# Optimization experiments

Hardware: AMD Instinct MI355X
Metric: run time of the kernel (lower is better)

## Reference

```python
import jax, jax.numpy as jnp
import numpy as np

B, LONG, SHORT, D, NH, HD = 512, 1000, 50, 64, 4, 16
NUM_ITEMS, TOPK = 100000, 50
NBUCKETS, HASHL, HASHD = 1024, 4, 16  # NOTE: 4 hash layers of D//4 so concat matches item_dim (source default 3 is a shape bug)


def lin(x, w, b):
    return x @ w.T + b


def ln(x, g, b):
    m = x.mean(-1, keepdims=True)
    v = ((x - m) ** 2).mean(-1, keepdims=True)
    return (x - m) / jnp.sqrt(v + 1e-5) * g + b


def setup_inputs() -> dict:
    key = jax.random.key(0)
    ks = jax.random.split(key, 24)
    rn = lambda i, s: jax.random.normal(ks[i], s, jnp.float32) * 0.02
    emb = rn(0, (NUM_ITEMS + 1, D)).at[0].set(0.0)  # padding_idx=0 row zeroed
    return dict(
        user_features=jax.random.normal(ks[1], (B, D), jnp.float32),
        target_item_id=jax.random.randint(ks[2], (B,), 0, NUM_ITEMS + 1),
        short_hist_ids=jax.random.randint(ks[3], (B, SHORT), 0, NUM_ITEMS + 1),
        long_hist_ids=jax.random.randint(ks[4], (B, LONG), 0, NUM_ITEMS + 1),
        item_emb=emb,
        tproj_w=rn(5, (D, D)), tproj_b=jnp.zeros((D,), jnp.float32),
        attn_w1=rn(6, (64, 3 * D)), attn_b1=jnp.zeros((64,), jnp.float32),
        attn_w2=rn(7, (1, 64)), attn_b2=jnp.zeros((1,), jnp.float32),
        hash_emb=rn(8, (HASHL, NBUCKETS, HASHD)),
        sdim_w=rn(9, (D, D)), sdim_b=jnp.zeros((D,), jnp.float32),
        tf_qkv_w=rn(10, (2, 3 * D, D)), tf_qkv_b=jnp.zeros((2, 3 * D), jnp.float32),
        tf_out_w=rn(11, (2, D, D)), tf_out_b=jnp.zeros((2, D), jnp.float32),
        tf_ln1_g=jnp.ones((2, D), jnp.float32), tf_ln1_b=jnp.zeros((2, D), jnp.float32),
        tf_ff1_w=rn(12, (2, 2 * D, D)), tf_ff1_b=jnp.zeros((2, 2 * D), jnp.float32),
        tf_ff2_w=rn(13, (2, D, 2 * D)), tf_ff2_b=jnp.zeros((2, D), jnp.float32),
        tf_ln2_g=jnp.ones((2, D), jnp.float32), tf_ln2_b=jnp.zeros((2, D), jnp.float32),
        fus_w1=rn(14, (256, 4 * D)), fus_b1=jnp.zeros((256,), jnp.float32),
        fus_w2=rn(15, (128, 256)), fus_b2=jnp.zeros((128,), jnp.float32),
        fus_w3=rn(16, (1, 128)), fus_b3=jnp.zeros((1,), jnp.float32),
    )


def sim_forward(user_features, item_emb, tproj_w, tproj_b, attn_w1, attn_b1,
                attn_w2, attn_b2, hash_emb, sdim_w, sdim_b, tf_qkv_w, tf_qkv_b,
                tf_out_w, tf_out_b, tf_ln1_g, tf_ln1_b, tf_ff1_w, tf_ff1_b,
                tf_ff2_w, tf_ff2_b, tf_ln2_g, tf_ln2_b, fus_w1, fus_b1, fus_w2,
                fus_b2, fus_w3, fus_b3, target_item_id, short_hist_ids, long_hist_ids):
    # target projection
    target_emb = lin(item_emb[target_item_id], tproj_w, tproj_b)         # [B,D]
    # ---- hard search over long history ----
    long_emb = item_emb[long_hist_ids]                                    # [B,L,D]
    t = jnp.broadcast_to(target_emb[:, None, :], long_emb.shape)
    cc = jnp.concatenate([t, long_emb, long_emb * t], axis=-1)            # [B,L,3D]
    scores = lin(jax.nn.relu(lin(cc, attn_w1, attn_b1)), attn_w2, attn_b2)[..., 0]
    attn = jax.nn.softmax(scores, axis=-1)                                # [B,L]
    top_w, top_i = jax.lax.top_k(attn, TOPK)
    top_w = jax.nn.softmax(top_w, axis=-1)
    top_e = jnp.take_along_axis(long_emb, top_i[..., None], axis=1)       # [B,K,D]
    hard_repr = (top_w[..., None] * top_e).sum(axis=1)                    # [B,D]
    # ---- SDIM soft search ----
    bucket = long_hist_ids % NBUCKETS
    h = hash_emb[:, bucket].mean(axis=2)                                  # [HL,B,HD]
    hash_repr = jnp.moveaxis(h, 0, 1).reshape(h.shape[1], HASHL * HASHD)  # [B,D]
    soft_repr = lin(hash_repr + long_emb.mean(axis=1), sdim_w, sdim_b)    # [B,D]
    # ---- BST transformer over short history (post-norm, relu, dropout=eval) ----
    x = item_emb[short_hist_ids]                                          # [B,S,D]
    for l in range(2):
        qkv = lin(x, tf_qkv_w[l], tf_qkv_b[l])
        q, k, v = jnp.split(qkv, 3, axis=-1)
        q = q.reshape(B, SHORT, NH, HD); k = k.reshape(B, SHORT, NH, HD); v = v.reshape(B, SHORT, NH, HD)
        sc = jnp.einsum('bqhd,bkhd->bhqk', q, k) / np.sqrt(HD).astype(np.float32)
        a = jax.nn.softmax(sc, axis=-1)
        o = jnp.einsum('bhqk,bkhd->bqhd', a, v).reshape(B, SHORT, D)
        x = ln(x + lin(o, tf_out_w[l], tf_out_b[l]), tf_ln1_g[l], tf_ln1_b[l])
        f = lin(jax.nn.relu(lin(x, tf_ff1_w[l], tf_ff1_b[l])), tf_ff2_w[l], tf_ff2_b[l])
        x = ln(x + f, tf_ln2_g[l], tf_ln2_b[l])
    bst_repr = x.mean(axis=1)                                             # [B,D]
    # ---- fusion MLP ----
    combined = jnp.concatenate([user_features, hard_repr, soft_repr, bst_repr], axis=-1)
    hdn = jax.nn.relu(lin(combined, fus_w1, fus_b1))
    hdn = jax.nn.relu(lin(hdn, fus_w2, fus_b2))
    return lin(hdn, fus_w3, fus_b3)[..., 0]                               # [B]


def reference(user_features, target_item_id, short_hist_ids, long_hist_ids,
              item_emb, tproj_w, tproj_b, attn_w1, attn_b1, attn_w2, attn_b2,
              hash_emb, sdim_w, sdim_b, tf_qkv_w, tf_qkv_b, tf_out_w, tf_out_b,
              tf_ln1_g, tf_ln1_b, tf_ff1_w, tf_ff1_b, tf_ff2_w, tf_ff2_b,
              tf_ln2_g, tf_ln2_b, fus_w1, fus_b1, fus_w2, fus_b2, fus_w3, fus_b3):
    return sim_forward(user_features, item_emb, tproj_w, tproj_b, attn_w1, attn_b1,
                       attn_w2, attn_b2, hash_emb, sdim_w, sdim_b, tf_qkv_w, tf_qkv_b,
                       tf_out_w, tf_out_b, tf_ln1_g, tf_ln1_b, tf_ff1_w, tf_ff1_b,
                       tf_ff2_w, tf_ff2_b, tf_ln2_g, tf_ln2_b, fus_w1, fus_b1,
                       fus_w2, fus_b2, fus_w3, fus_b3, target_item_id,
                       short_hist_ids, long_hist_ids)
```

## Files before the change

kernel.cpp:

```cpp
#include <hip/hip_runtime.h>
#include <math.h>

#define NB 512
#define LONGN 1000
#define SHORTN 50
#define TOPKN 50
#define HALFN 500
#define NG 8
#define EROW 72
#define BROW 72
#define F1ROW 136

typedef __attribute__((ext_vector_type(8))) short bf16x8;
typedef __attribute__((ext_vector_type(4))) float f32x4;

__device__ __forceinline__ float dot4(float4 a, float4 b) {
  return a.x*b.x + a.y*b.y + a.z*b.z + a.w*b.w;
}

template<int N>
__device__ __forceinline__ float dotN(const float* w, const float* x) {
  const float4* w4 = (const float4*)w;
  const float4* x4 = (const float4*)x;
  float a0 = 0.f, a1 = 0.f, a2 = 0.f, a3 = 0.f;
  #pragma unroll
  for (int k = 0; k < N/4; k += 4) {
    a0 += dot4(w4[k],   x4[k]);
    a1 += dot4(w4[k+1], x4[k+1]);
    a2 += dot4(w4[k+2], x4[k+2]);
    a3 += dot4(w4[k+3], x4[k+3]);
  }
  return (a0 + a1) + (a2 + a3);
}

__device__ __forceinline__ float wave_sum(float v) {
  #pragma unroll
  for (int off = 32; off > 0; off >>= 1) v += __shfl_xor(v, off);
  return v;
}
__device__ __forceinline__ float wave_max(float v) {
  #pragma unroll
  for (int off = 32; off > 0; off >>= 1) v = fmaxf(v, __shfl_xor(v, off));
  return v;
}

__device__ __forceinline__ unsigned short f2bf(float x) {
  unsigned u = __float_as_uint(x);
  return (unsigned short)((u + 0x7fffu + ((u >> 16) & 1u)) >> 16);
}

__global__ __launch_bounds__(256, 3) void hard_scores_kernel(
    const int* __restrict__ target_item_id,
    const int* __restrict__ long_hist_ids,
    const float* __restrict__ item_emb,
    const float* __restrict__ tproj_w, const float* __restrict__ tproj_b,
    const float* __restrict__ attn_w1, const float* __restrict__ attn_b1,
    const float* __restrict__ attn_w2, const float* __restrict__ attn_b2,
    const float* __restrict__ hash_emb,
    float* __restrict__ scores_ws, float* __restrict__ partA,
    float* __restrict__ partH)
{
  __shared__ __align__(16) short Abf[64*EROW];
  __shared__ __align__(16) short Ebuf[2][64*EROW];
  __shared__ __align__(16) float tv[64];
  __shared__ __align__(16) float te[64];
  __shared__ __align__(16) float2 cw[64];
  __shared__ int idsL[HALFN];
  __shared__ __align__(16) float redE[4*64];

  const int bid = blockIdx.x;
  const int b = bid >> 1, half = bid & 1;
  const int base = half * HALFN;
  const int tid = threadIdx.x;
  const int wid = tid >> 6, lane = tid & 63;

  if (tid < 64) tv[tid] = item_emb[target_item_id[b]*64 + tid];
  for (int l = tid; l < HALFN; l += 256) idsL[l] = long_hist_ids[b*LONGN + base + l];
  __syncthreads();
  if (tid < 64) te[tid] = tproj_b[tid] + dotN<64>(tproj_w + tid*64, tv);
  __syncthreads();
  if (tid < 64) {
    float c = attn_b1[tid] + dotN<64>(attn_w1 + tid*192, te);
    cw[tid] = make_float2(c, attn_w2[tid]);
  }
  for (int idx = tid; idx < 4096; idx += 256) {
    int i = idx >> 6, j = idx & 63;
    Abf[i*EROW + j] = (short)f2bf(attn_w1[i*192 + 64 + j] + attn_w1[i*192 + 128 + j]*te[j]);
  }
  __syncthreads();

  bf16x8 a00,a01,a10,a11,a20,a21,a30,a31;
  {
    const short* ap = Abf + (lane & 15)*EROW + ((lane >> 4) << 3);
    a00 = *(const bf16x8*)(ap +  0*EROW);  a01 = *(const bf16x8*)(ap +  0*EROW + 32);
    a10 = *(const bf16x8*)(ap + 16*EROW);  a11 = *(const bf16x8*)(ap + 16*EROW + 32);
    a20 = *(const bf16x8*)(ap + 32*EROW);  a21 = *(const bf16x8*)(ap + 32*EROW + 32);
    a30 = *(const bf16x8*)(ap + 48*EROW);  a31 = *(const bf16x8*)(ap + 48*EROW + 32);
  }

  const float b2s = attn_b2[0];
  const int it_g = tid >> 2;
  const int dimg = (tid & 3) * 16;

  float4 sE0 = {0,0,0,0}, sE1 = {0,0,0,0}, sE2 = {0,0,0,0}, sE3 = {0,0,0,0};

  {
    const float4* ep = (const float4*)(item_emb + (size_t)idsL[it_g]*64 + dimg);
    float4 r0 = ep[0], r1 = ep[1], r2 = ep[2], r3 = ep[3];
    sE0.x+=r0.x; sE0.y+=r0.y; sE0.z+=r0.z; sE0.w+=r0.w;
    sE1.x+=r1.x; sE1.y+=r1.y; sE1.z+=r1.z; sE1.w+=r1.w;
    sE2.x+=r2.x; sE2.y+=r2.y; sE2.z+=r2.z; sE2.w+=r2.w;
    sE3.x+=r3.x; sE3.y+=r3.y; sE3.z+=r3.z; sE3.w+=r3.w;
    bf16x8 w0, w1;
    w0[0]=(short)f2bf(r0.x); w0[1]=(short)f2bf(r0.y); w0[2]=(short)f2bf(r0.z); w0[3]=(short)f2bf(r0.w);
    w0[4]=(short)f2bf(r1.x); w0[5]=(short)f2bf(r1.y); w0[6]=(short)f2bf(r1.z); w0[7]=(short)f2bf(r1.w);
    w1[0]=(short)f2bf(r2.x); w1[1]=(short)f2bf(r2.y); w1[2]=(short)f2bf(r2.z); w1[3]=(short)f2bf(r2.w);
    w1[4]=(short)f2bf(r3.x); w1[5]=(short)f2bf(r3.y); w1[6]=(short)f2bf(r3.z); w1[7]=(short)f2bf(r3.w);
    short* dst = &Ebuf[0][it_g*EROW + dimg];
    *(bf16x8*)dst = w0;  *(bf16x8*)(dst + 8) = w1;
  }
  __syncthreads();

  int buf = 0;
  for (int g = 0; g < NG; ++g) {
    float4 r0={0,0,0,0}, r1={0,0,0,0}, r2={0,0,0,0}, r3={0,0,0,0};
    const bool more = (g + 1 < NG);
    if (more) {
      const int gi = (g+1)*64 + it_g;
      if (gi < HALFN) {
        const float4* ep = (const float4*)(item_emb + (size_t)idsL[gi]*64 + dimg);
        r0 = ep[0]; r1 = ep[1]; r2 = ep[2]; r3 = ep[3];
      }
    }

    f32x4 acc0={0,0,0,0}, acc1={0,0,0,0}, acc2={0,0,0,0}, acc3={0,0,0,0};
    {
      const short* ep = &Ebuf[buf][(wid*16 + (lane & 15))*EROW + ((lane >> 4) << 3)];
      bf16x8 b0 = *(const bf16x8*)(ep);
      bf16x8 b1 = *(const bf16x8*)(ep + 32);
      acc0 = __builtin_amdgcn_mfma_f32_16x16x32_bf16(a00, b0, acc0, 0, 0, 0);
      acc0 = __builtin_amdgcn_mfma_f32_16x16x32_bf16(a01, b1, acc0, 0, 0, 0);
      acc1 = __builtin_amdgcn_mfma_f32_16x16x32_bf16(a10, b0, acc1, 0, 0, 0);
      acc1 = __builtin_amdgcn_mfma_f32_16x16x32_bf16(a11, b1, acc1, 0, 0, 0);
      acc2 = __builtin_amdgcn_mfma_f32_16x16x32_bf16(a20, b0, acc2, 0, 0, 0);
      acc2 = __builtin_amdgcn_mfma_f32_16x16x32_bf16(a21, b1, acc2, 0, 0, 0);
      acc3 = __builtin_amdgcn_mfma_f32_16x16x32_bf16(a30, b0, acc3, 0, 0, 0);
      acc3 = __builtin_amdgcn_mfma_f32_16x16x32_bf16(a31, b1, acc3, 0, 0, 0);
    }
    float p = 0.f;
    {
      const int rbase = (lane >> 4) << 2;
      #pragma unroll
      for (int r = 0; r < 4; ++r) {
        float2 c0 = cw[ 0 + rbase + r];
        float2 c1 = cw[16 + rbase + r];
        float2 c2 = cw[32 + rbase + r];
        float2 c3 = cw[48 + rbase + r];
        p += c0.y * fmaxf(acc0[r] + c0.x, 0.f);
        p += c1.y * fmaxf(acc1[r] + c1.x, 0.f);
        p += c2.y * fmaxf(acc2[r] + c2.x, 0.f);
        p += c3.y * fmaxf(acc3[r] + c3.x, 0.f);
      }
    }
    p += __shfl_xor(p, 16);
    p += __shfl_xor(p, 32);
    if (lane < 16) {
      const int gi = g*64 + wid*16 + lane;
      if (gi < HALFN) scores_ws[b*LONGN + base + gi] = b2s + p;
    }

    if (more) {
      sE0.x+=r0.x; sE0.y+=r0.y; sE0.z+=r0.z; sE0.w+=r0.w;
      sE1.x+=r1.x; sE1.y+=r1.y; sE1.z+=r1.z; sE1.w+=r1.w;
      sE2.x+=r2.x; sE2.y+=r2.y; sE2.z+=r2.z; sE2.w+=r2.w;
      sE3.x+=r3.x; sE3.y+=r3.y; sE3.z+=r3.z; sE3.w+=r3.w;
      bf16x8 w0, w1;
      w0[0]=(short)f2bf(r0.x); w0[1]=(short)f2bf(r0.y); w0[2]=(short)f2bf(r0.z); w0[3]=(short)f2bf(r0.w);
      w0[4]=(short)f2bf(r1.x); w0[5]=(short)f2bf(r1.y); w0[6]=(short)f2bf(r1.z); w0[7]=(short)f2bf(r1.w);
      w1[0]=(short)f2bf(r2.x); w1[1]=(short)f2bf(r2.y); w1[2]=(short)f2bf(r2.z); w1[3]=(short)f2bf(r2.w);
      w1[4]=(short)f2bf(r3.x); w1[5]=(short)f2bf(r3.y); w1[6]=(short)f2bf(r3.z); w1[7]=(short)f2bf(r3.w);
      short* dst = &Ebuf[buf ^ 1][it_g*EROW + dimg];
      *(bf16x8*)dst = w0;  *(bf16x8*)(dst + 8) = w1;
    }
    __syncthreads();
    buf ^= 1;
  }

  {
    float* red = (float*)&Ebuf[0][0];
    const int b17 = tid * 17;
    red[b17+ 0]=sE0.x; red[b17+ 1]=sE0.y; red[b17+ 2]=sE0.z; red[b17+ 3]=sE0.w;
    red[b17+ 4]=sE1.x; red[b17+ 5]=sE1.y; red[b17+ 6]=sE1.z; red[b17+ 7]=sE1.w;
    red[b17+ 8]=sE2.x; red[b17+ 9]=sE2.y; red[b17+10]=sE2.z; red[b17+11]=sE2.w;
    red[b17+12]=sE3.x; red[b17+13]=sE3.y; red[b17+14]=sE3.z; red[b17+15]=sE3.w;
    __syncthreads();
    if (tid < 64) {
      const int dg = tid >> 4, dw = tid & 15;
      float s = 0.f;
      for (int j = 0; j < 64; ++j) s += red[(j*4 + dg)*17 + dw];
      partA[bid*64 + tid] = s;
    }
  }

  {
    const int hl = lane >> 4, dd = lane & 15;
    const float* hb = hash_emb + hl*1024*16 + dd;
    float accH = 0.f;
    for (int l = wid; l < HALFN; l += 4)
      accH += hb[(idsL[l] & 1023)*16];
    redE[wid*64 + lane] = accH;
  }
  __syncthreads();
  if (wid == 0)
    partH[bid*64 + lane] = redE[lane] + redE[64+lane] + redE[128+lane] + redE[192+lane];
}

__global__ __launch_bounds__(256) void hard_finish_kernel(
    const int* __restrict__ long_hist_ids,
    const float* __restrict__ item_emb,
    const float* __restrict__ sdim_w, const float* __restrict__ sdim_b,
    const float* __restrict__ scores_ws,
    const float* __restrict__ partA, const float* __restrict__ partH,
    float* __restrict__ hard_out, float* __restrict__ soft_out)
{
  __shared__ __align__(16) float scores[LONGN];
  __shared__ int   idsL[LONGN];
  __shared__ __align__(16) unsigned long long kv[1024];
  __shared__ __align__(16) float redE[4*64];
  __shared__ __align__(16) float vecbuf[64];
  __shared__ float redV[4];
  __shared__ float selV[TOPKN];
  __shared__ int   selI[TOPKN];

  const int b = blockIdx.x;
  const int tid = threadIdx.x;
  const int wid = tid >> 6, lane = tid & 63;

  for (int l = tid; l < LONGN; l += 256) {
    scores[l] = scores_ws[b*LONGN + l];
    idsL[l] = long_hist_ids[b*LONGN + l];
  }
  __syncthreads();

  if (tid < 64)
    vecbuf[tid] = (partA[(2*b)*64 + tid] + partA[(2*b+1)*64 + tid]
                 + partH[(2*b)*64 + tid] + partH[(2*b+1)*64 + tid]) * (1.f/1000.f);
  __syncthreads();
  if (tid < 64)
    soft_out[b*64 + tid] = sdim_b[tid] + dotN<64>(sdim_w + tid*64, vecbuf);

  float mx = -INFINITY;
  for (int l = tid; l < LONGN; l += 256) mx = fmaxf(mx, scores[l]);
  mx = wave_max(mx);
  if (lane == 0) redV[wid] = mx;
  __syncthreads();
  mx = fmaxf(fmaxf(redV[0], redV[1]), fmaxf(redV[2], redV[3]));
  __syncthreads();
  float sm = 0.f;
  for (int l = tid; l < LONGN; l += 256) {
    float a = expf(scores[l] - mx);
    scores[l] = a;
    sm += a;
  }
  sm = wave_sum(sm);
  if (lane == 0) redV[wid] = sm;
  __syncthreads();
  {
    const float inv = 1.f / (redV[0] + redV[1] + redV[2] + redV[3]);
    for (int l = tid; l < LONGN; l += 256) scores[l] *= inv;
  }
  __syncthreads();

  for (int l = tid; l < 1024; l += 256) {
    if (l < LONGN) {
      unsigned vb = __float_as_uint(scores[l]);
      kv[l] = ((unsigned long long)(~vb) << 32) | (unsigned)l;
    } else {
      kv[l] = 0xFFFFFFFFFFFFFFFFull;
    }
  }
  __syncthreads();

  for (int k = 2; k <= 1024; k <<= 1) {
    for (int j = k >> 1; j > 0; j >>= 1) {
      #pragma unroll 2
      for (int p = tid; p < 512; p += 256) {
        const int i = ((p & ~(j-1)) << 1) | (p & (j-1));
        const int m = i + j;
        const bool up = ((i & k) == 0);
        unsigned long long a = kv[i], c = kv[m];
        if ((a > c) == up) { kv[i] = c; kv[m] = a; }
      }
      __syncthreads();
    }
  }

  if (tid < TOPKN) {
    unsigned long long key = kv[tid];
    selI[tid] = (int)(unsigned)(key & 0xFFFFFFFFu);
    selV[tid] = __uint_as_float(~(unsigned)(key >> 32));
  }
  __syncthreads();

  if (wid == 0) {
    float v = (lane < TOPKN) ? selV[lane] : -INFINITY;
    float m2 = wave_max(v);
    float e = (lane < TOPKN) ? expf(v - m2) : 0.f;
    float s2 = wave_sum(e);
    if (lane < TOPKN) selV[lane] = e / s2;
  }
  __syncthreads();

  float accR = 0.f;
  for (int r = wid; r < TOPKN; r += 4)
    accR += selV[r] * item_emb[idsL[selI[r]]*64 + lane];
  redE[wid*64 + lane] = accR;
  __syncthreads();
  if (wid == 0)
    hard_out[b*64 + lane] = redE[lane] + redE[64+lane] + redE[128+lane] + redE[192+lane];
}

__global__ __launch_bounds__(256) void bst_prep_kernel(
    const float* __restrict__ qkv_w, const float* __restrict__ out_w,
    const float* __restrict__ ff1_w, const float* __restrict__ ff2_w,
    short* __restrict__ wF)
{
  const int t = blockIdx.x*256 + threadIdx.x;
  if (t >= 8192) return;
  const int fid = t >> 6, lane = t & 63;
  const int n16 = lane & 15, k8 = (lane >> 4) * 8;
  const float* src;
  if (fid < 48)      { int f=fid,    l=f/24, r=f%24, nt=r>>1, kc=r&1;
    src = qkv_w + l*12288 + (nt*16+n16)*64 + kc*32 + k8; }
  else if (fid < 64) { int f=fid-48, l=f>>3, r=f&7,  nt=r>>1, kc=r&1;
    src = out_w + l*4096 + (nt*16+n16)*64 + kc*32 + k8; }
  else if (fid < 96) { int f=fid-64, l=f>>4, r=f&15, nt=r>>1, kc=r&1;
    src = ff1_w + l*8192 + (nt*16+n16)*64 + kc*32 + k8; }
  else               { int f=fid-96, l=f>>4, r=f&15, nt=r>>2, kc=r&3;
    src = ff2_w + l*8192 + (nt*16+n16)*128 + kc*32 + k8; }
  short* dst = wF + fid*512 + lane*8;
  #pragma unroll
  for (int j = 0; j < 8; ++j) dst[j] = (short)f2bf(src[j]);
}

__global__ __launch_bounds__(256) void bst_kernel(
    const int* __restrict__ short_ids, const float* __restrict__ item_emb,
    const short* __restrict__ wF,
    const float* __restrict__ qkv_b, const float* __restrict__ out_b,
    const float* __restrict__ ln1_g, const float* __restrict__ ln1_b,
    const float* __restrict__ ff1_b, const float* __restrict__ ff2_b,
    const float* __restrict__ ln2_g, const float* __restrict__ ln2_b,
    float* __restrict__ bst_out)
{
  __shared__ __align__(16) float xf[SHORTN*64];
  __shared__ __align__(16) short xbf[64*BROW];
  __shared__ __align__(16) float qf[SHORTN*68];
  __shared__ __align__(16) float arena[SHORTN*132];
  __shared__ __align__(16) short obf[64*BROW];

  short* f1bf = (short*)arena;

  const int b = blockIdx.x, tid = threadIdx.x;
  const int wid = tid >> 6, lane = tid & 63;
  const int n16 = lane & 15;
  const int kg8 = (lane >> 4) << 3;
  const int mrow = (lane >> 4) << 2;

  for (int idx = tid; idx < SHORTN*64; idx += 256) {
    int s = idx >> 6, j = idx & 63;
    float v = item_emb[short_ids[b*SHORTN + s]*64 + j];
    xf[idx] = v;
    xbf[s*BROW + j] = (short)f2bf(v);
  }
  for (int idx = tid; idx < 14*BROW; idx += 256) {
    xbf[50*BROW + idx] = 0;
    obf[50*BROW + idx] = 0;
  }
  __syncthreads();

  for (int l = 0; l < 2; ++l) {
    {
      const short* ap = xbf + n16*BROW + kg8;
      bf16x8 A00 = *(const bf16x8*)(ap);            bf16x8 A01 = *(const bf16x8*)(ap + 32);
      bf16x8 A10 = *(const bf16x8*)(ap + 16*BROW);  bf16x8 A11 = *(const bf16x8*)(ap + 16*BROW + 32);
      bf16x8 A20 = *(const bf16x8*)(ap + 32*BROW);  bf16x8 A21 = *(const bf16x8*)(ap + 32*BROW + 32);
      bf16x8 A30 = *(const bf16x8*)(ap + 48*BROW);  bf16x8 A31 = *(const bf16x8*)(ap + 48*BROW + 32);
      #pragma unroll
      for (int t = 0; t < 3; ++t) {
        const int nt = wid*3 + t;
        const short* bp = wF + (size_t)(l*24 + nt*2)*512 + lane*8;
        bf16x8 B0 = *(const bf16x8*)(bp);
        bf16x8 B1 = *(const bf16x8*)(bp + 512);
        f32x4 c0={0,0,0,0}, c1={0,0,0,0}, c2={0,0,0,0}, c3={0,0,0,0};
        c0 = __builtin_amdgcn_mfma_f32_16x16x32_bf16(A00, B0, c0, 0,0,0);
        c0 = __builtin_amdgcn_mfma_f32_16x16x32_bf16(A01, B1, c0, 0,0,0);
        c1 = __builtin_amdgcn_mfma_f32_16x16x32_bf16(A10, B0, c1, 0,0,0);
        c1 = __builtin_amdgcn_mfma_f32_16x16x32_bf16(A11, B1, c1, 0,0,0);
        c2 = __builtin_amdgcn_mfma_f32_16x16x32_bf16(A20, B0, c2, 0,0,0);
        c2 = __builtin_amdgcn_mfma_f32_16x16x32_bf16(A21, B1, c2, 0,0,0);
        c3 = __builtin_amdgcn_mfma_f32_16x16x32_bf16(A30, B0, c3, 0,0,0);
        c3 = __builtin_amdgcn_mfma_f32_16x16x32_bf16(A31, B1, c3, 0,0,0);
        const int c = nt*16 + n16;
        const float bias = qkv_b[l*192 + c];
        #pragma unroll
        for (int r = 0; r < 4; ++r) {
          int m0 = mrow + r;
          float v0 = c0[r] + bias;
          float v1 = c1[r] + bias;
          float v2 = c2[r] + bias;
          float v3 = c3[r] + bias;
          if (c < 64) {
            qf[m0*68 + c] = v0;
            if (m0+16 < SHORTN) qf[(m0+16)*68 + c] = v1;
            if (m0+32 < SHORTN) qf[(m0+32)*68 + c] = v2;
            if (m0+48 < SHORTN) qf[(m0+48)*68 + c] = v3;
          } else {
            const int cc = c - 64;
            arena[m0*132 + cc] = v0;
            if (m0+16 < SHORTN) arena[(m0+16)*132 + cc] = v1;
            if (m0+32 < SHORTN) arena[(m0+32)*132 + cc] = v2;
            if (m0+48 < SHORTN) arena[(m0+48)*132 + cc] = v3;
          }
        }
      }
    }
    __syncthreads();

    if (tid < 4*SHORTN) {
      const int h = tid / SHORTN, s = tid - h*SHORTN;
      const float4* qp = (const float4*)(qf + s*68 + h*16);
      const float4 qA = qp[0], qB2 = qp[1], qC = qp[2], qD = qp[3];
      float m = -INFINITY, ss = 0.f;
      float4 oa0 = {0,0,0,0}, oa1 = {0,0,0,0}, oa2 = {0,0,0,0}, oa3 = {0,0,0,0};
      for (int t2 = 0; t2 < SHORTN; ++t2) {
        const float4* kp = (const float4*)(arena + t2*132 + h*16);
        float d = dot4(qA,kp[0]) + dot4(qB2,kp[1]) + dot4(qC,kp[2]) + dot4(qD,kp[3]);
        d *= 0.25f;
        float mn = fmaxf(m, d);
        float al = __expf(m - mn);
        float a  = __expf(d - mn);
        m = mn;
        ss = ss*al + a;
        const float4* vp = (const float4*)(arena + t2*132 + 64 + h*16);
        float4 v0 = vp[0], v1 = vp[1], v2 = vp[2], v3 = vp[3];
        oa0.x = oa0.x*al + a*v0.x; oa0.y = oa0.y*al + a*v0.y;
        oa0.z = oa0.z*al + a*v0.z; oa0.w = oa0.w*al + a*v0.w;
        oa1.x = oa1.x*al + a*v1.x; oa1.y = oa1.y*al + a*v1.y;
        oa1.z = oa1.z*al + a*v1.z; oa1.w = oa1.w*al + a*v1.w;
        oa2.x = oa2.x*al + a*v2.x; oa2.y = oa2.y*al + a*v2.y;
        oa2.z = oa2.z*al + a*v2.z; oa2.w = oa2.w*al + a*v2.w;
        oa3.x = oa3.x*al + a*v3.x; oa3.y = oa3.y*al + a*v3.y;
        oa3.z = oa3.z*al + a*v3.z; oa3.w = oa3.w*al + a*v3.w;
      }
      const float inv = 1.f/ss;
      bf16x8 w0, w1;
      w0[0]=(short)f2bf(oa0.x*inv); w0[1]=(short)f2bf(oa0.y*inv);
      w0[2]=(short)f2bf(oa0.z*inv); w0[3]=(short)f2bf(oa0.w*inv);
      w0[4]=(short)f2bf(oa1.x*inv); w0[5]=(short)f2bf(oa1.y*inv);
      w0[6]=(short)f2bf(oa1.z*inv); w0[7]=(short)f2bf(oa1.w*inv);
      w1[0]=(short)f2bf(oa2.x*inv); w1[1]=(short)f2bf(oa2.y*inv);
      w1[2]=(short)f2bf(oa2.z*inv); w1[3]=(short)f2bf(oa2.w*inv);
      w1[4]=(short)f2bf(oa3.x*inv); w1[5]=(short)f2bf(oa3.y*inv);
      w1[6]=(short)f2bf(oa3.z*inv); w1[7]=(short)f2bf(oa3.w*inv);
      short* op = obf + s*BROW + h*16;
      *(bf16x8*)op = w0;  *(bf16x8*)(op + 8) = w1;
    }
    __syncthreads();

    {
      const short* ap = obf + n16*BROW + kg8;
      bf16x8 A00 = *(const bf16x8*)(ap);            bf16x8 A01 = *(const bf16x8*)(ap + 32);
      bf16x8 A10 = *(const bf16x8*)(ap + 16*BROW);  bf16x8 A11 = *(const bf16x8*)(ap + 16*BROW + 32);
      bf16x8 A20 = *(const bf16x8*)(ap + 32*BROW);  bf16x8 A21 = *(const bf16x8*)(ap + 32*BROW + 32);
      bf16x8 A30 = *(const bf16x8*)(ap + 48*BROW);  bf16x8 A31 = *(const bf16x8*)(ap + 48*BROW + 32);
      const int nt = wid;
      const short* bp = wF + (size_t)(48 + l*8 + nt*2)*512 + lane*8;
      bf16x8 B0 = *(const bf16x8*)(bp);
      bf16x8 B1 = *(const bf16x8*)(bp + 512);
      f32x4 c0={0,0,0,0}, c1={0,0,0,0}, c2={0,0,0,0}, c3={0,0,0,0};
      c0 = __builtin_amdgcn_mfma_f32_16x16x32_bf16(A00, B0, c0, 0,0,0);
      c0 = __builtin_amdgcn_mfma_f32_16x16x32_bf16(A01, B1, c0, 0,0,0);
      c1 = __builtin_amdgcn_mfma_f32_16x16x32_bf16(A10, B0, c1, 0,0,0);
      c1 = __builtin_amdgcn_mfma_f32_16x16x32_bf16(A11, B1, c1, 0,0,0);
      c2 = __builtin_amdgcn_mfma_f32_16x16x32_bf16(A20, B0, c2, 0,0,0);
      c2 = __builtin_amdgcn_mfma_f32_16x16x32_bf16(A21, B1, c2, 0,0,0);
      c3 = __builtin_amdgcn_mfma_f32_16x16x32_bf16(A30, B0, c3, 0,0,0);
      c3 = __builtin_amdgcn_mfma_f32_16x16x32_bf16(A31, B1, c3, 0,0,0);
      const int c = nt*16 + n16;
      const float bias = out_b[l*64 + c];
      #pragma unroll
      for (int r = 0; r < 4; ++r) {
        int m0 = mrow + r;
        arena[m0*68 + c] = xf[m0*64 + c] + bias + c0[r];
        if (m0+16 < SHORTN) arena[(m0+16)*68 + c] = xf[(m0+16)*64 + c] + bias + c1[r];
        if (m0+32 < SHORTN) arena[(m0+32)*68 + c] = xf[(m0+32)*64 + c] + bias + c2[r];
        if (m0+48 < SHORTN) arena[(m0+48)*68 + c] = xf[(m0+48)*64 + c] + bias + c3[r];
      }
      for (int idx = tid; idx < 14*F1ROW; idx += 256) f1bf[50*F1ROW + idx] = 0;
    }
    __syncthreads();

    {
      const float g = ln1_g[l*64 + lane], bb = ln1_b[l*64 + lane];
      for (int s = wid; s < SHORTN; s += 4) {
        float y = arena[s*68 + lane];
        float mean = wave_sum(y) * (1.f/64.f);
        float dv = y - mean;
        float var = wave_sum(dv*dv) * (1.f/64.f);
        float r = dv / sqrtf(var + 1e-5f) * g + bb;
        xf[s*64 + lane] = r;
        xbf[s*BROW + lane] = (short)f2bf(r);
      }
    }
    __syncthreads();

    {
      const short* ap = xbf + n16*BROW + kg8;
      bf16x8 A00 = *(const bf16x8*)(ap);            bf16x8 A01 = *(const bf16x8*)(ap + 32);
      bf16x8 A10 = *(const bf16x8*)(ap + 16*BROW);  bf16x8 A11 = *(const bf16x8*)(ap + 16*BROW + 32);
      bf16x8 A20 = *(const bf16x8*)(ap + 32*BROW);  bf16x8 A21 = *(const bf16x8*)(ap + 32*BROW + 32);
      bf16x8 A30 = *(const bf16x8*)(ap + 48*BROW);  bf16x8 A31 = *(const bf16x8*)(ap + 48*BROW + 32);
      #pragma unroll
      for (int t = 0; t < 2; ++t) {
        const int nt = wid*2 + t;
        const short* bp = wF + (size_t)(64 + l*16 + nt*2)*512 + lane*8;
        bf16x8 B0 = *(const bf16x8*)(bp);
        bf16x8 B1 = *(const bf16x8*)(bp + 512);
        f32x4 c0={0,0,0,0}, c1={0,0,0,0}, c2={0,0,0,0}, c3={0,0,0,0};
        c0 = __builtin_amdgcn_mfma_f32_16x16x32_bf16(A00, B0, c0, 0,0,0);
        c0 = __builtin_amdgcn_mfma_f32_16x16x32_bf16(A01, B1, c0, 0,0,0);
        c1 = __builtin_amdgcn_mfma_f32_16x16x32_bf16(A10, B0, c1, 0,0,0);
        c1 = __builtin_amdgcn_mfma_f32_16x16x32_bf16(A11, B1, c1, 0,0,0);
        c2 = __builtin_amdgcn_mfma_f32_16x16x32_bf16(A20, B0, c2, 0,0,0);
        c2 = __builtin_amdgcn_mfma_f32_16x16x32_bf16(A21, B1, c2, 0,0,0);
        c3 = __builtin_amdgcn_mfma_f32_16x16x32_bf16(A30, B0, c3, 0,0,0);
        c3 = __builtin_amdgcn_mfma_f32_16x16x32_bf16(A31, B1, c3, 0,0,0);
        const int c = nt*16 + n16;
        const float bias = ff1_b[l*128 + c];
        #pragma unroll
        for (int r = 0; r < 4; ++r) {
          int m0 = mrow + r;
          f1bf[m0*F1ROW + c] = (short)f2bf(fmaxf(c0[r] + bias, 0.f));
          if (m0+16 < SHORTN) f1bf[(m0+16)*F1ROW + c] = (short)f2bf(fmaxf(c1[r] + bias, 0.f));
          if (m0+32 < SHORTN) f1bf[(m0+32)*F1ROW + c] = (short)f2bf(fmaxf(c2[r] + bias, 0.f));
          if (m0+48 < SHORTN) f1bf[(m0+48)*F1ROW + c] = (short)f2bf(fmaxf(c3[r] + bias, 0.f));
        }
      }
    }
    __syncthreads();

    {
      const int nt = wid;
      f32x4 c0={0,0,0,0}, c1={0,0,0,0}, c2={0,0,0,0}, c3={0,0,0,0};
      #pragma unroll
      for (int kc = 0; kc < 4; ++kc) {
        const short* ap = f1bf + n16*F1ROW + kc*32 + kg8;
        bf16x8 A0 = *(const bf16x8*)(ap);
        bf16x8 A1 = *(const bf16x8*)(ap + 16*F1ROW);
        bf16x8 A2 = *(const bf16x8*)(ap + 32*F1ROW);
        bf16x8 A3 = *(const bf16x8*)(ap + 48*F1ROW);
        const short* bp = wF + (size_t)(96 + l*16 + nt*4 + kc)*512 + lane*8;
        bf16x8 B = *(const bf16x8*)(bp);
        c0 = __builtin_amdgcn_mfma_f32_16x16x32_bf16(A0, B, c0, 0,0,0);
        c1 = __builtin_amdgcn_mfma_f32_16x16x32_bf16(A1, B, c1, 0,0,0);
        c2 = __builtin_amdgcn_mfma_f32_16x16x32_bf16(A2, B, c2, 0,0,0);
        c3 = __builtin_amdgcn_mfma_f32_16x16x32_bf16(A3, B, c3, 0,0,0);
      }
      __syncthreads();
      const int c = nt*16 + n16;
      const float bias = ff2_b[l*64 + c];
      #pragma unroll
      for (int r = 0; r < 4; ++r) {
        int m0 = mrow + r;
        arena[m0*68 + c] = xf[m0*64 + c] + bias + c0[r];
        if (m0+16 < SHORTN) arena[(m0+16)*68 + c] = xf[(m0+16)*64 + c] + bias + c1[r];
        if (m0+32 < SHORTN) arena[(m0+32)*68 + c] = xf[(m0+32)*64 + c] + bias + c2[r];
        if (m0+48 < SHORTN) arena[(m0+48)*68 + c] = xf[(m0+48)*64 + c] + bias + c3[r];
      }
    }
    __syncthreads();

    {
      const float g = ln2_g[l*64 + lane], bb = ln2_b[l*64 + lane];
      for (int s = wid; s < SHORTN; s += 4) {
        float y = arena[s*68 + lane];
        float mean = wave_sum(y) * (1.f/64.f);
        float dv = y - mean;
        float var = wave_sum(dv*dv) * (1.f/64.f);
        float r = dv / sqrtf(var + 1e-5f) * g + bb;
        xf[s*64 + lane] = r;
        xbf[s*BROW + lane] = (short)f2bf(r);
      }
    }
    __syncthreads();
  }

  float acc = 0.f;
  for (int s = wid; s < SHORTN; s += 4) acc += xf[s*64 + lane];
  qf[wid*64 + lane] = acc;
  __syncthreads();
  if (wid == 0)
    bst_out[b*64 + lane] = (qf[lane] + qf[64+lane] + qf[128+lane] + qf[192+lane]) * (1.f/50.f);
}

__global__ __launch_bounds__(256) void fusion_kernel(
    const float* __restrict__ user, const float* __restrict__ hard,
    const float* __restrict__ soft, const float* __restrict__ bst,
    const float* __restrict__ w1, const float* __restrict__ b1,
    const float* __restrict__ w2, const float* __restrict__ b2,
    const float* __restrict__ w3, const float* __restrict__ b3,
    float* __restrict__ out)
{
  __shared__ __align__(16) float comb[256];
  __shared__ __align__(16) float h1[256];
  __shared__ __align__(16) float h2[128];
  const int b = blockIdx.x, tid = threadIdx.x;
  if (tid < 64)       comb[tid] = user[b*64 + tid];
  else if (tid < 128) comb[tid] = hard[b*64 + tid - 64];
  else if (tid < 192) comb[tid] = soft[b*64 + tid - 128];
  else                comb[tid] = bst[b*64 + tid - 192];
  __syncthreads();
  h1[tid] = fmaxf(b1[tid] + dotN<256>(w1 + tid*256, comb), 0.f);
  __syncthreads();
  if (tid < 128) h2[tid] = fmaxf(b2[tid] + dotN<256>(w2 + tid*256, h1), 0.f);
  __syncthreads();
  if (tid < 64) {
    float p = w3[tid]*h2[tid] + w3[tid+64]*h2[tid+64];
    p = wave_sum(p);
    if (tid == 0) out[b] = p + b3[0];
  }
}

extern "C" void kernel_launch(void* const* d_in, const int* in_sizes, int n_in,
                              void* d_out, int out_size, void* d_ws, size_t ws_size,
                              hipStream_t stream) {
  const float* user_features  = (const float*)d_in[0];
  const int*   target_item_id = (const int*)  d_in[1];
  const int*   short_hist_ids = (const int*)  d_in[2];
  const int*   long_hist_ids  = (const int*)  d_in[3];
  const float* item_emb       = (const float*)d_in[4];
  const float* tproj_w  = (const float*)d_in[5];
  const float* tproj_b  = (const float*)d_in[6];
  const float* attn_w1  = (const float*)d_in[7];
  const float* attn_b1  = (const float*)d_in[8];
  const float* attn_w2  = (const float*)d_in[9];
  const float* attn_b2  = (const float*)d_in[10];
  const float* hash_emb = (const float*)d_in[11];
  const float* sdim_w   = (const float*)d_in[12];
  const float* sdim_b   = (const float*)d_in[13];
  const float* tf_qkv_w = (const float*)d_in[14];
  const float* tf_qkv_b = (const float*)d_in[15];
  const float* tf_out_w = (const float*)d_in[16];
  const float* tf_out_b = (const float*)d_in[17];
  const float* tf_ln1_g = (const float*)d_in[18];
  const float* tf_ln1_b = (const float*)d_in[19];
  const float* tf_ff1_w = (const float*)d_in[20];
  const float* tf_ff1_b = (const float*)d_in[21];
  const float* tf_ff2_w = (const float*)d_in[22];
  const float* tf_ff2_b = (const float*)d_in[23];
  const float* tf_ln2_g = (const float*)d_in[24];
  const float* tf_ln2_b = (const float*)d_in[25];
  const float* fus_w1   = (const float*)d_in[26];
  const float* fus_b1   = (const float*)d_in[27];
  const float* fus_w2   = (const float*)d_in[28];
  const float* fus_b2   = (const float*)d_in[29];
  const float* fus_w3   = (const float*)d_in[30];
  const float* fus_b3   = (const float*)d_in[31];

  float* ws = (float*)d_ws;
  float* hard = ws;
  float* soft = hard + NB*64;
  float* bst  = soft + NB*64;
  float* scores_ws = bst + NB*64;
  float* partA = scores_ws + NB*LONGN;
  float* partH = partA + NB*2*64;
  short* wF    = (short*)(partH + NB*2*64);

  bst_prep_kernel<<<32, 256, 0, stream>>>(tf_qkv_w, tf_out_w, tf_ff1_w, tf_ff2_w, wF);
  hard_scores_kernel<<<2*NB, 256, 0, stream>>>(target_item_id, long_hist_ids,
      item_emb, tproj_w, tproj_b, attn_w1, attn_b1, attn_w2, attn_b2,
      hash_emb, scores_ws, partA, partH);
  hard_finish_kernel<<<NB, 256, 0, stream>>>(long_hist_ids, item_emb,
      sdim_w, sdim_b, scores_ws, partA, partH, hard, soft);
  bst_kernel<<<NB, 256, 0, stream>>>(short_hist_ids, item_emb, wF,
      tf_qkv_b, tf_out_b, tf_ln1_g, tf_ln1_b, tf_ff1_b, tf_ff2_b,
      tf_ln2_g, tf_ln2_b, bst);
  fusion_kernel<<<NB, 256, 0, stream>>>(user_features, hard, soft, bst,
      fus_w1, fus_b1, fus_w2, fus_b2, fus_w3, fus_b3, (float*)d_out);
}
```

Measured before the change: 173.0 us.

## Merge hard-score and BST kernels into one heterogeneous launch

Combines hard_scores_kernel and bst_kernel into a single main_kernel whose blocks dispatch by blockIdx%3: two of every three blocks run the long-history scoring path and one runs the short-history transformer path. Shared memory becomes a dynamic union sized to the larger struct. This removes one launch and lets the two independent workloads overlap on the GPU instead of running back to back. In exchange, every block reserves the larger (BST) LDS footprint, and the hard path loses its launch_bounds(256,3) occupancy hint, which may reduce occupancy for the scoring blocks.

After: 223.3 us. +29.0%, slower.

```diff
diff --git a/kernel.cpp b/kernel.cpp
--- a/kernel.cpp
+++ b/kernel.cpp
@@ -49,7 +49,25 @@
   return (unsigned short)((u + 0x7fffu + ((u >> 16) & 1u)) >> 16);
 }
 
-__global__ __launch_bounds__(256, 3) void hard_scores_kernel(
+struct __align__(16) HardSM {
+  short Abf[64*EROW];
+  short Ebuf[2][64*EROW];
+  float tv[64];
+  float te[64];
+  float2 cw[64];
+  int idsL[HALFN];
+  float redE[4*64];
+};
+struct __align__(16) BstSM {
+  float xf[SHORTN*64];
+  short xbf[64*BROW];
+  float qf[SHORTN*68];
+  float arena[SHORTN*132];
+  short obf[64*BROW];
+};
+
+__device__ void hard_scores_path(
+    const int bid, HardSM* S,
     const int* __restrict__ target_item_id,
     const int* __restrict__ long_hist_ids,
     const float* __restrict__ item_emb,
@@ -60,38 +78,29 @@
     float* __restrict__ scores_ws, float* __restrict__ partA,
     float* __restrict__ partH)
 {
-  __shared__ __align__(16) short Abf[64*EROW];
-  __shared__ __align__(16) short Ebuf[2][64*EROW];
-  __shared__ __align__(16) float tv[64];
-  __shared__ __align__(16) float te[64];
-  __shared__ __align__(16) float2 cw[64];
-  __shared__ int idsL[HALFN];
-  __shared__ __align__(16) float redE[4*64];
-
-  const int bid = blockIdx.x;
   const int b = bid >> 1, half = bid & 1;
   const int base = half * HALFN;
   const int tid = threadIdx.x;
   const int wid = tid >> 6, lane = tid & 63;
 
-  if (tid < 64) tv[tid] = item_emb[target_item_id[b]*64 + tid];
-  for (int l = tid; l < HALFN; l += 256) idsL[l] = long_hist_ids[b*LONGN + base + l];
-  __syncthreads();
-  if (tid < 64) te[tid] = tproj_b[tid] + dotN<64>(tproj_w + tid*64, tv);
+  if (tid < 64) S->tv[tid] = item_emb[target_item_id[b]*64 + tid];
+  for (int l = tid; l < HALFN; l += 256) S->idsL[l] = long_hist_ids[b*LONGN + base + l];
+  __syncthreads();
+  if (tid < 64) S->te[tid] = tproj_b[tid] + dotN<64>(tproj_w + tid*64, S->tv);
   __syncthreads();
   if (tid < 64) {
-    float c = attn_b1[tid] + dotN<64>(attn_w1 + tid*192, te);
-    cw[tid] = make_float2(c, attn_w2[tid]);
+    float c = attn_b1[tid] + dotN<64>(attn_w1 + tid*192, S->te);
+    S->cw[tid] = make_float2(c, attn_w2[tid]);
   }
   for (int idx = tid; idx < 4096; idx += 256) {
     int i = idx >> 6, j = idx & 63;
-    Abf[i*EROW + j] = (short)f2bf(attn_w1[i*192 + 64 + j] + attn_w1[i*192 + 128 + j]*te[j]);
+    S->Abf[i*EROW + j] = (short)f2bf(attn_w1[i*192 + 64 + j] + attn_w1[i*192 + 128 + j]*S->te[j]);
   }
   __syncthreads();
 
   bf16x8 a00,a01,a10,a11,a20,a21,a30,a31;
   {
-    const short* ap = Abf + (lane & 15)*EROW + ((lane >> 4) << 3);
+    const short* ap = S->Abf + (lane & 15)*EROW + ((lane >> 4) << 3);
     a00 = *(const bf16x8*)(ap +  0*EROW);  a01 = *(const bf16x8*)(ap +  0*EROW + 32);
     a10 = *(const bf16x8*)(ap + 16*EROW);  a11 = *(const bf16x8*)(ap + 16*EROW + 32);
     a20 = *(const bf16x8*)(ap + 32*EROW);  a21 = *(const bf16x8*)(ap + 32*EROW + 32);
@@ -105,7 +114,7 @@
   float4 sE0 = {0,0,0,0}, sE1 = {0,0,0,0}, sE2 = {0,0,0,0}, sE3 = {0,0,0,0};
 
   {
-    const float4* ep = (const float4*)(item_emb + (size_t)idsL[it_g]*64 + dimg);
+    const float4* ep = (const float4*)(item_emb + (size_t)S->idsL[it_g]*64 + dimg);
     float4 r0 = ep[0], r1 = ep[1], r2 = ep[2], r3 = ep[3];
     sE0.x+=r0.x; sE0.y+=r0.y; sE0.z+=r0.z; sE0.w+=r0.w;
     sE1.x+=r1.x; sE1.y+=r1.y; sE1.z+=r1.z; sE1.w+=r1.w;
@@ -116,7 +125,7 @@
     w0[4]=(short)f2bf(r1.x); w0[5]=(short)f2bf(r1.y); w0[6]=(short)f2bf(r1.z); w0[7]=(short)f2bf(r1.w);
     w1[0]=(short)f2bf(r2.x); w1[1]=(short)f2bf(r2.y); w1[2]=(short)f2bf(r2.z); w1[3]=(short)f2bf(r2.w);
     w1[4]=(short)f2bf(r3.x); w1[5]=(short)f2bf(r3.y); w1[6]=(short)f2bf(r3.z); w1[7]=(short)f2bf(r3.w);
-    short* dst = &Ebuf[0][it_g*EROW + dimg];
+    short* dst = &S->Ebuf[0][it_g*EROW + dimg];
     *(bf16x8*)dst = w0;  *(bf16x8*)(dst + 8) = w1;
   }
   __syncthreads();
@@ -128,14 +137,14 @@
     if (more) {
       const int gi = (g+1)*64 + it_g;
       if (gi < HALFN) {
-        const float4* ep = (const float4*)(item_emb + (size_t)idsL[gi]*64 + dimg);
+        const float4* ep = (const float4*)(item_emb + (size_t)S->idsL[gi]*64 + dimg);
         r0 = ep[0]; r1 = ep[1]; r2 = ep[2]; r3 = ep[3];
       }
     }
 
     f32x4 acc0={0,0,0,0}, acc1={0,0,0,0}, acc2={0,0,0,0}, acc3={0,0,0,0};
     {
-      const short* ep = &Ebuf[buf][(wid*16 + (lane & 15))*EROW + ((lane >> 4) << 3)];
+      const short* ep = &S->Ebuf[buf][(wid*16 + (lane & 15))*EROW + ((lane >> 4) << 3)];
       bf16x8 b0 = *(const bf16x8*)(ep);
       bf16x8 b1 = *(const bf16x8*)(ep + 32);
       acc0 = __builtin_amdgcn_mfma_f32_16x16x32_bf16(a00, b0, acc0, 0, 0, 0);
@@ -152,10 +161,10 @@
       const int rbase = (lane >> 4) << 2;
       #pragma unroll
       for (int r = 0; r < 4; ++r) {
-        float2 c0 = cw[ 0 + rbase + r];
-        float2 c1 = cw[16 + rbase + r];
-        float2 c2 = cw[32 + rbase + r];
-        float2 c3 = cw[48 + rbase + r];
+        float2 c0 = S->cw[ 0 + rbase + r];
+        float2 c1 = S->cw[16 + rbase + r];
+        float2 c2 = S->cw[32 + rbase + r];
+        float2 c3 = S->cw[48 + rbase + r];
         p += c0.y * fmaxf(acc0[r] + c0.x, 0.f);
         p += c1.y * fmaxf(acc1[r] + c1.x, 0.f);
         p += c2.y * fmaxf(acc2[r] + c2.x, 0.f);
@@ -179,7 +188,7 @@
       w0[4]=(short)f2bf(r1.x); w0[5]=(short)f2bf(r1.y); w0[6]=(short)f2bf(r1.z); w0[7]=(short)f2bf(r1.w);
       w1[0]=(short)f2bf(r2.x); w1[1]=(short)f2bf(r2.y); w1[2]=(short)f2bf(r2.z); w1[3]=(short)f2bf(r2.w);
       w1[4]=(short)f2bf(r3.x); w1[5]=(short)f2bf(r3.y); w1[6]=(short)f2bf(r3.z); w1[7]=(short)f2bf(r3.w);
-      short* dst = &Ebuf[buf ^ 1][it_g*EROW + dimg];
+      short* dst = &S->Ebuf[buf ^ 1][it_g*EROW + dimg];
       *(bf16x8*)dst = w0;  *(bf16x8*)(dst + 8) = w1;
     }
     __syncthreads();
@@ -187,7 +196,7 @@
   }
 
   {
-    float* red = (float*)&Ebuf[0][0];
+    float* red = (float*)&S->Ebuf[0][0];
     const int b17 = tid * 17;
     red[b17+ 0]=sE0.x; red[b17+ 1]=sE0.y; red[b17+ 2]=sE0.z; red[b17+ 3]=sE0.w;
     red[b17+ 4]=sE1.x; red[b17+ 5]=sE1.y; red[b17+ 6]=sE1.z; red[b17+ 7]=sE1.w;
@@ -207,143 +216,16 @@
     const float* hb = hash_emb + hl*1024*16 + dd;
     float accH = 0.f;
     for (int l = wid; l < HALFN; l += 4)
-      accH += hb[(idsL[l] & 1023)*16];
-    redE[wid*64 + lane] = accH;
+      accH += hb[(S->idsL[l] & 1023)*16];
+    S->redE[wid*64 + lane] = accH;
   }
   __syncthreads();
   if (wid == 0)
-    partH[bid*64 + lane] = redE[lane] + redE[64+lane] + redE[128+lane] + redE[192+lane];
-}
-
-__global__ __launch_bounds__(256) void hard_finish_kernel(
-    const int* __restrict__ long_hist_ids,
-    const float* __restrict__ item_emb,
-    const float* __restrict__ sdim_w, const float* __restrict__ sdim_b,
-    const float* __restrict__ scores_ws,
-    const float* __restrict__ partA, const float* __restrict__ partH,
-    float* __restrict__ hard_out, float* __restrict__ soft_out)
-{
-  __shared__ __align__(16) float scores[LONGN];
-  __shared__ int   idsL[LONGN];
-  __shared__ __align__(16) unsigned long long kv[1024];
-  __shared__ __align__(16) float redE[4*64];
-  __shared__ __align__(16) float vecbuf[64];
-  __shared__ float redV[4];
-  __shared__ float selV[TOPKN];
-  __shared__ int   selI[TOPKN];
-
-  const int b = blockIdx.x;
-  const int tid = threadIdx.x;
-  const int wid = tid >> 6, lane = tid & 63;
-
-  for (int l = tid; l < LONGN; l += 256) {
-    scores[l] = scores_ws[b*LONGN + l];
-    idsL[l] = long_hist_ids[b*LONGN + l];
-  }
-  __syncthreads();
-
-  if (tid < 64)
-    vecbuf[tid] = (partA[(2*b)*64 + tid] + partA[(2*b+1)*64 + tid]
-                 + partH[(2*b)*64 + tid] + partH[(2*b+1)*64 + tid]) * (1.f/1000.f);
-  __syncthreads();
-  if (tid < 64)
-    soft_out[b*64 + tid] = sdim_b[tid] + dotN<64>(sdim_w + tid*64, vecbuf);
-
-  float mx = -INFINITY;
-  for (int l = tid; l < LONGN; l += 256) mx = fmaxf(mx, scores[l]);
-  mx = wave_max(mx);
-  if (lane == 0) redV[wid] = mx;
-  __syncthreads();
-  mx = fmaxf(fmaxf(redV[0], redV[1]), fmaxf(redV[2], redV[3]));
-  __syncthreads();
-  float sm = 0.f;
-  for (int l = tid; l < LONGN; l += 256) {
-    float a = expf(scores[l] - mx);
-    scores[l] = a;
-    sm += a;
-  }
-  sm = wave_sum(sm);
-  if (lane == 0) redV[wid] = sm;
-  __syncthreads();
-  {
-    const float inv = 1.f / (redV[0] + redV[1] + redV[2] + redV[3]);
-    for (int l = tid; l < LONGN; l += 256) scores[l] *= inv;
-  }
-  __syncthreads();
-
-  for (int l = tid; l < 1024; l += 256) {
-    if (l < LONGN) {
-      unsigned vb = __float_as_uint(scores[l]);
-      kv[l] = ((unsigned long long)(~vb) << 32) | (unsigned)l;
-    } else {
-      kv[l] = 0xFFFFFFFFFFFFFFFFull;
-    }
-  }
-  __syncthreads();
-
-  for (int k = 2; k <= 1024; k <<= 1) {
-    for (int j = k >> 1; j > 0; j >>= 1) {
-      #pragma unroll 2
-      for (int p = tid; p < 512; p += 256) {
-        const int i = ((p & ~(j-1)) << 1) | (p & (j-1));
-        const int m = i + j;
-        const bool up = ((i & k) == 0);
-        unsigned long long a = kv[i], c = kv[m];
-        if ((a > c) == up) { kv[i] = c; kv[m] = a; }
-      }
-      __syncthreads();
-    }
-  }
-
-  if (tid < TOPKN) {
-    unsigned long long key = kv[tid];
-    selI[tid] = (int)(unsigned)(key & 0xFFFFFFFFu);
-    selV[tid] = __uint_as_float(~(unsigned)(key >> 32));
-  }
-  __syncthreads();
-
-  if (wid == 0) {
-    float v = (lane < TOPKN) ? selV[lane] : -INFINITY;
-    float m2 = wave_max(v);
-    float e = (lane < TOPKN) ? expf(v - m2) : 0.f;
-    float s2 = wave_sum(e);
-    if (lane < TOPKN) selV[lane] = e / s2;
-  }
-  __syncthreads();
-
-  float accR = 0.f;
-  for (int r = wid; r < TOPKN; r += 4)
-    accR += selV[r] * item_emb[idsL[selI[r]]*64 + lane];
-  redE[wid*64 + lane] = accR;
-  __syncthreads();
-  if (wid == 0)
-    hard_out[b*64 + lane] = redE[lane] + redE[64+lane] + redE[128+lane] + redE[192+lane];
-}
-
-__global__ __launch_bounds__(256) void bst_prep_kernel(
-    const float* __restrict__ qkv_w, const float* __restrict__ out_w,
-    const float* __restrict__ ff1_w, const float* __restrict__ ff2_w,
-    short* __restrict__ wF)
-{
-  const int t = blockIdx.x*256 + threadIdx.x;
-  if (t >= 8192) return;
-  const int fid = t >> 6, lane = t & 63;
-  const int n16 = lane & 15, k8 = (lane >> 4) * 8;
-  const float* src;
-  if (fid < 48)      { int f=fid,    l=f/24, r=f%24, nt=r>>1, kc=r&1;
-    src = qkv_w + l*12288 + (nt*16+n16)*64 + kc*32 + k8; }
-  else if (fid < 64) { int f=fid-48, l=f>>3, r=f&7,  nt=r>>1, kc=r&1;
-    src = out_w + l*4096 + (nt*16+n16)*64 + kc*32 + k8; }
-  else if (fid < 96) { int f=fid-64, l=f>>4, r=f&15, nt=r>>1, kc=r&1;
-    src = ff1_w + l*8192 + (nt*16+n16)*64 + kc*32 + k8; }
-  else               { int f=fid-96, l=f>>4, r=f&15, nt=r>>2, kc=r&3;
-    src = ff2_w + l*8192 + (nt*16+n16)*128 + kc*32 + k8; }
-  short* dst = wF + fid*512 + lane*8;
-  #pragma unroll
-  for (int j = 0; j < 8; ++j) dst[j] = (short)f2bf(src[j]);
-}
-
-__global__ __launch_bounds__(256) void bst_kernel(
+    partH[bid*64 + lane] = S->redE[lane] + S->redE[64+lane] + S->redE[128+lane] + S->redE[192+lane];
+}
+
+__device__ void bst_path(
+    const int b, BstSM* S,
     const int* __restrict__ short_ids, const float* __restrict__ item_emb,
     const short* __restrict__ wF,
     const float* __restrict__ qkv_b, const float* __restrict__ out_b,
@@ -352,15 +234,14 @@
     const float* __restrict__ ln2_g, const float* __restrict__ ln2_b,
     float* __restrict__ bst_out)
 {
-  __shared__ __align__(16) float xf[SHORTN*64];
-  __shared__ __align__(16) short xbf[64*BROW];
-  __shared__ __align__(16) float qf[SHORTN*68];
-  __shared__ __align__(16) float arena[SHORTN*132];
-  __shared__ __align__(16) short obf[64*BROW];
-
-  short* f1bf = (short*)arena;
-
-  const int b = blockIdx.x, tid = threadIdx.x;
+  float* xf    = S->xf;
+  short* xbf   = S->xbf;
+  float* qf    = S->qf;
+  float* arena = S->arena;
+  short* obf   = S->obf;
+  short* f1bf  = (short*)arena;
+
+  const int tid = threadIdx.x;
   const int wid = tid >> 6, lane = tid & 63;
   const int n16 = lane & 15;
   const int kg8 = (lane >> 4) << 3;
@@ -603,6 +484,166 @@
     bst_out[b*64 + lane] = (qf[lane] + qf[64+lane] + qf[128+lane] + qf[192+lane]) * (1.f/50.f);
 }
 
+__global__ __launch_bounds__(256) void main_kernel(
+    const int* __restrict__ target_item_id,
+    const int* __restrict__ long_hist_ids,
+    const int* __restrict__ short_hist_ids,
+    const float* __restrict__ item_emb,
+    const float* __restrict__ tproj_w, const float* __restrict__ tproj_b,
+    const float* __restrict__ attn_w1, const float* __restrict__ attn_b1,
+    const float* __restrict__ attn_w2, const float* __restrict__ attn_b2,
+    const float* __restrict__ hash_emb,
+    const short* __restrict__ wF,
+    const float* __restrict__ qkv_b, const float* __restrict__ out_b,
+    const float* __restrict__ ln1_g, const float* __restrict__ ln1_b,
+    const float* __restrict__ ff1_b, const float* __restrict__ ff2_b,
+    const float* __restrict__ ln2_g, const float* __restrict__ ln2_b,
+    float* __restrict__ scores_ws, float* __restrict__ partA,
+    float* __restrict__ partH, float* __restrict__ bst_out)
+{
+  extern __shared__ __align__(16) char smraw[];
+  const int blk = blockIdx.x;
+  const int r3 = blk % 3;
+  if (r3 < 2) {
+    hard_scores_path((blk/3)*2 + r3, (HardSM*)smraw,
+        target_item_id, long_hist_ids, item_emb, tproj_w, tproj_b,
+        attn_w1, attn_b1, attn_w2, attn_b2, hash_emb,
+        scores_ws, partA, partH);
+  } else {
+    bst_path(blk/3, (BstSM*)smraw,
+        short_hist_ids, item_emb, wF, qkv_b, out_b,
+        ln1_g, ln1_b, ff1_b, ff2_b, ln2_g, ln2_b, bst_out);
+  }
+}
+
+__global__ __launch_bounds__(256) void hard_finish_kernel(
+    const int* __restrict__ long_hist_ids,
+    const float* __restrict__ item_emb,
+    const float* __restrict__ sdim_w, const float* __restrict__ sdim_b,
+    const float* __restrict__ scores_ws,
+    const float* __restrict__ partA, const float* __restrict__ partH,
+    float* __restrict__ hard_out, float* __restrict__ soft_out)
+{
+  __shared__ __align__(16) float scores[LONGN];
+  __shared__ int   idsL[LONGN];
+  __shared__ __align__(16) unsigned long long kv[1024];
+  __shared__ __align__(16) float redE[4*64];
+  __shared__ __align__(16) float vecbuf[64];
+  __shared__ float redV[4];
+  __shared__ float selV[TOPKN];
+  __shared__ int   selI[TOPKN];
+
+  const int b = blockIdx.x;
+  const int tid = threadIdx.x;
+  const int wid = tid >> 6, lane = tid & 63;
+
+  for (int l = tid; l < LONGN; l += 256) {
+    scores[l] = scores_ws[b*LONGN + l];
+    idsL[l] = long_hist_ids[b*LONGN + l];
+  }
+  __syncthreads();
+
+  if (tid < 64)
+    vecbuf[tid] = (partA[(2*b)*64 + tid] + partA[(2*b+1)*64 + tid]
+                 + partH[(2*b)*64 + tid] + partH[(2*b+1)*64 + tid]) * (1.f/1000.f);
+  __syncthreads();
+  if (tid < 64)
+    soft_out[b*64 + tid] = sdim_b[tid] + dotN<64>(sdim_w + tid*64, vecbuf);
+
+  float mx = -INFINITY;
+  for (int l = tid; l < LONGN; l += 256) mx = fmaxf(mx, scores[l]);
+  mx = wave_max(mx);
+  if (lane == 0) redV[wid] = mx;
+  __syncthreads();
+  mx = fmaxf(fmaxf(redV[0], redV[1]), fmaxf(redV[2], redV[3]));
+  __syncthreads();
+  float sm = 0.f;
+  for (int l = tid; l < LONGN; l += 256) {
+    float a = expf(scores[l] - mx);
+    scores[l] = a;
+    sm += a;
+  }
+  sm = wave_sum(sm);
+  if (lane == 0) redV[wid] = sm;
+  __syncthreads();
+  {
+    const float inv = 1.f / (redV[0] + redV[1] + redV[2] + redV[3]);
+    for (int l = tid; l < LONGN; l += 256) scores[l] *= inv;
+  }
+  __syncthreads();
+
+  for (int l = tid; l < 1024; l += 256) {
+    if (l < LONGN) {
+      unsigned vb = __float_as_uint(scores[l]);
+      kv[l] = ((unsigned long long)(~vb) << 32) | (unsigned)l;
+    } else {
+      kv[l] = 0xFFFFFFFFFFFFFFFFull;
+    }
+  }
+  __syncthreads();
+
+  for (int k = 2; k <= 1024; k <<= 1) {
+    for (int j = k >> 1; j > 0; j >>= 1) {
+      #pragma unroll 2
+      for (int p = tid; p < 512; p += 256) {
+        const int i = ((p & ~(j-1)) << 1) | (p & (j-1));
+        const int m = i + j;
+        const bool up = ((i & k) == 0);
+        unsigned long long a = kv[i], c = kv[m];
+        if ((a > c) == up) { kv[i] = c; kv[m] = a; }
+      }
+      __syncthreads();
+    }
+  }
+
+  if (tid < TOPKN) {
+    unsigned long long key = kv[tid];
+    selI[tid] = (int)(unsigned)(key & 0xFFFFFFFFu);
+    selV[tid] = __uint_as_float(~(unsigned)(key >> 32));
+  }
+  __syncthreads();
+
+  if (wid == 0) {
+    float v = (lane < TOPKN) ? selV[lane] : -INFINITY;
+    float m2 = wave_max(v);
+    float e = (lane < TOPKN) ? expf(v - m2) : 0.f;
+    float s2 = wave_sum(e);
+    if (lane < TOPKN) selV[lane] = e / s2;
+  }
+  __syncthreads();
+
+  float accR = 0.f;
+  for (int r = wid; r < TOPKN; r += 4)
+    accR += selV[r] * item_emb[idsL[selI[r]]*64 + lane];
+  redE[wid*64 + lane] = accR;
+  __syncthreads();
+  if (wid == 0)
+    hard_out[b*64 + lane] = redE[lane] + redE[64+lane] + redE[128+lane] + redE[192+lane];
+}
+
+__global__ __launch_bounds__(256) void bst_prep_kernel(
+    const float* __restrict__ qkv_w, const float* __restrict__ out_w,
+    const float* __restrict__ ff1_w, const float* __restrict__ ff2_w,
+    short* __restrict__ wF)
+{
+  const int t = blockIdx.x*256 + threadIdx.x;
+  if (t >= 8192) return;
+  const int fid = t >> 6, lane = t & 63;
+  const int n16 = lane & 15, k8 = (lane >> 4) * 8;
+  const float* src;
+  if (fid < 48)      { int f=fid,    l=f/24, r=f%24, nt=r>>1, kc=r&1;
+    src = qkv_w + l*12288 + (nt*16+n16)*64 + kc*32 + k8; }
+  else if (fid < 64) { int f=fid-48, l=f>>3, r=f&7,  nt=r>>1, kc=r&1;
+    src = out_w + l*4096 + (nt*16+n16)*64 + kc*32 + k8; }
+  else if (fid < 96) { int f=fid-64, l=f>>4, r=f&15, nt=r>>1, kc=r&1;
+    src = ff1_w + l*8192 + (nt*16+n16)*64 + kc*32 + k8; }
+  else               { int f=fid-96, l=f>>4, r=f&15, nt=r>>2, kc=r&3;
+    src = ff2_w + l*8192 + (nt*16+n16)*128 + kc*32 + k8; }
+  short* dst = wF + fid*512 + lane*8;
+  #pragma unroll
+  for (int j = 0; j < 8; ++j) dst[j] = (short)f2bf(src[j]);
+}
+
 __global__ __launch_bounds__(256) void fusion_kernel(
     const float* __restrict__ user, const float* __restrict__ hard,
     const float* __restrict__ soft, const float* __restrict__ bst,
@@ -676,15 +717,18 @@
   float* partH = partA + NB*2*64;
   short* wF    = (short*)(partH + NB*2*64);
 
+  constexpr size_t lds_bytes =
+      sizeof(BstSM) > sizeof(HardSM) ? sizeof(BstSM) : sizeof(HardSM);
+
   bst_prep_kernel<<<32, 256, 0, stream>>>(tf_qkv_w, tf_out_w, tf_ff1_w, tf_ff2_w, wF);
-  hard_scores_kernel<<<2*NB, 256, 0, stream>>>(target_item_id, long_hist_ids,
-      item_emb, tproj_w, tproj_b, attn_w1, attn_b1, attn_w2, attn_b2,
-      hash_emb, scores_ws, partA, partH);
+  main_kernel<<<3*NB, 256, lds_bytes, stream>>>(
+      target_item_id, long_hist_ids, short_hist_ids, item_emb,
+      tproj_w, tproj_b, attn_w1, attn_b1, attn_w2, attn_b2, hash_emb,
+      wF, tf_qkv_b, tf_out_b, tf_ln1_g, tf_ln1_b, tf_ff1_b, tf_ff2_b,
+      tf_ln2_g, tf_ln2_b,
+      scores_ws, partA, partH, bst);
   hard_finish_kernel<<<NB, 256, 0, stream>>>(long_hist_ids, item_emb,
       sdim_w, sdim_b, scores_ws, partA, partH, hard, soft);
-  bst_kernel<<<NB, 256, 0, stream>>>(short_hist_ids, item_emb, wF,
-      tf_qkv_b, tf_out_b, tf_ln1_g, tf_ln1_b, tf_ff1_b, tf_ff2_b,
-      tf_ln2_g, tf_ln2_b, bst);
   fusion_kernel<<<NB, 256, 0, stream>>>(user_features, hard, soft, bst,
       fus_w1, fus_b1, fus_w2, fus_b2, fus_w3, fus_b3, (float*)d_out);
 }
```
